# Optimization experiments

Measured on AMD Instinct MI355X. Metric: run time of the kernel, lower is better.

The kernel has to match this reference:

```python
import jax, jax.numpy as jnp
import numpy as np

N = 2048      # number of nodes (batch_size in original code)
D = 128       # node feature dim (fea_shape)
R = 43        # number of relation types (rel_weight = Linear(43, 1))


def setup_inputs() -> dict:
    key = jax.random.key(0)
    ks = jax.random.split(key, 9)
    inputs   = jax.random.normal(ks[0], (N, D), dtype=jnp.float32)
    relation = jax.random.normal(ks[1], (N, N, R), dtype=jnp.float32)
    rel_mask = jax.random.normal(ks[2], (N, N), dtype=jnp.float32)
    s_rel  = 1.0 / np.sqrt(R)
    s_feat = 1.0 / np.sqrt(D)
    w_rel  = jax.random.uniform(ks[3], (R, 1), jnp.float32, -s_rel, s_rel)
    b_rel  = jax.random.uniform(ks[4], (1,),   jnp.float32, -s_rel, s_rel)
    w_head = jax.random.uniform(ks[5], (D, 1), jnp.float32, -s_feat, s_feat)
    b_head = jax.random.uniform(ks[6], (1,),   jnp.float32, -s_feat, s_feat)
    w_tail = jax.random.uniform(ks[7], (D, 1), jnp.float32, -s_feat, s_feat)
    b_tail = jax.random.uniform(ks[8], (1,),   jnp.float32, -s_feat, s_feat)
    return dict(inputs=inputs, relation=relation, rel_mask=rel_mask,
                w_rel=w_rel, b_rel=b_rel, w_head=w_head, b_head=b_head,
                w_tail=w_tail, b_tail=b_tail)


def reference(inputs, relation, rel_mask, w_rel, b_rel, w_head, b_head, w_tail, b_tail):
    # rel_weight = Linear(43,1)(relation)[:, :, -1]  -> [N, N]
    rel_w = jnp.einsum('ijr,r->ij', relation, w_rel[:, 0]) + b_rel[0]
    # head @ ones^T + ones @ tail^T  == broadcast outer-sum  -> [N, N]
    head = inputs @ w_head + b_head          # [N, 1]
    tail = inputs @ w_tail + b_tail          # [N, 1]
    weight = head + tail.T + rel_w           # [N, N]
    # masked softmax over dim=0 (rows), then weighted aggregation
    weight_masked = jax.nn.softmax(rel_mask + weight, axis=0)
    return weight_masked @ inputs            # [N, D]
```

## Files before the change

kernel.cpp:

```cpp
#include <hip/hip_runtime.h>
#include <math.h>

#define N 2048
#define D 128
#define R 43
#define SPLIT 8
#define CHUNKS 32

typedef const __attribute__((address_space(1))) void* as1_cptr;
typedef __attribute__((address_space(3))) void* as3_ptr;

__global__ __launch_bounds__(256) void k_headtail(
    const float* __restrict__ inputs,
    const float* __restrict__ w_head, const float* __restrict__ b_head,
    const float* __restrict__ w_tail, const float* __restrict__ b_tail,
    float* __restrict__ head, float* __restrict__ tail)
{
    const int t = threadIdx.x;
    const int row = blockIdx.x * 64 + (t >> 2);
    const int q = t & 3;
    const float4* rp = (const float4*)(inputs + (size_t)row * D + q * 32);
    const float4* wh = (const float4*)(w_head + q * 32);
    const float4* wt = (const float4*)(w_tail + q * 32);
    float h = 0.f, tl = 0.f;
    #pragma unroll
    for (int k = 0; k < 8; ++k) {
        float4 v = rp[k];
        float4 a = wh[k];
        float4 b = wt[k];
        h  += v.x * a.x + v.y * a.y + v.z * a.z + v.w * a.w;
        tl += v.x * b.x + v.y * b.y + v.z * b.z + v.w * b.w;
    }
    h  += __shfl_xor(h, 1);  h  += __shfl_xor(h, 2);
    tl += __shfl_xor(tl, 1); tl += __shfl_xor(tl, 2);
    if (q == 0) {
        head[row] = h  + b_head[0];
        tail[row] = tl + b_tail[0];
    }
}

__global__ __launch_bounds__(256) void k_scores(
    const float* __restrict__ rel, const float* __restrict__ rel_mask,
    const float* __restrict__ w_rel, const float* __restrict__ b_rel,
    const float* __restrict__ head, const float* __restrict__ tail,
    float* __restrict__ s)
{
    __shared__ float lds[2 * 256 * R];
    const int t    = threadIdx.x;
    const int lane = t & 63;
    const int wave = t >> 6;
    const int k0 = wave * 11;
    const int k1 = (wave == 3) ? 43 : (k0 + 11);

    float w[R];
    #pragma unroll
    for (int r = 0; r < R; ++r) w[r] = w_rel[r];
    const float brel = b_rel[0];

    char* lbase = (char*)lds;
    const int c0 = blockIdx.x * 64;

    {
        const char* src = (const char*)rel + (size_t)c0 * 44032;
        for (int k = k0; k < k1; ++k)
            __builtin_amdgcn_global_load_lds(
                (as1_cptr)(src + k * 1024 + lane * 16),
                (as3_ptr)(lbase + k * 1024), 16, 0, 0);
    }

    int cur = 0;
    for (int tt = 0; tt < 64; ++tt) {
        __syncthreads();

        if (tt < 63) {
            const char* src = (const char*)rel + (size_t)(c0 + tt + 1) * 44032;
            char* dst = lbase + (cur ^ 1) * 44032;
            for (int k = k0; k < k1; ++k)
                __builtin_amdgcn_global_load_lds(
                    (as1_cptr)(src + k * 1024 + lane * 16),
                    (as3_ptr)(dst + k * 1024), 16, 0, 0);
        }

        const size_t p = (size_t)(c0 + tt) * 256 + t;
        const int i = (int)(p >> 11);
        const int j = (int)(p & (N - 1));
        const float hd = head[i];
        const float tl = tail[j];
        const float mk = rel_mask[p];

        const float* b = lds + cur * (256 * R) + t * R;
        float a0 = 0.f, a1 = 0.f, a2 = 0.f, a3 = 0.f;
        #pragma unroll
        for (int r = 0; r < 40; r += 4) {
            a0 += b[r]     * w[r];
            a1 += b[r + 1] * w[r + 1];
            a2 += b[r + 2] * w[r + 2];
            a3 += b[r + 3] * w[r + 3];
        }
        a0 += b[40] * w[40];
        a1 += b[41] * w[41];
        a2 += b[42] * w[42];

        s[p] = brel + ((a0 + a1) + (a2 + a3)) + hd + tl + mk;
        cur ^= 1;
    }
}

__global__ __launch_bounds__(256) void k_colstats_part(
    const float* __restrict__ s, float* __restrict__ mpart, float* __restrict__ lpart)
{
    const int j = (blockIdx.x & 7) * 256 + threadIdx.x;
    const int c = blockIdx.x >> 3;
    const int i0 = c * 64;
    float mx = -1e30f;
    for (int i = i0; i < i0 + 64; ++i)
        mx = fmaxf(mx, s[(size_t)i * N + j]);
    float sum = 0.f;
    for (int i = i0; i < i0 + 64; ++i)
        sum += __expf(s[(size_t)i * N + j] - mx);
    mpart[c * N + j] = mx;
    lpart[c * N + j] = sum;
}

__global__ __launch_bounds__(256) void k_colstats_comb(
    const float* __restrict__ mpart, const float* __restrict__ lpart,
    float* __restrict__ m, float* __restrict__ rl)
{
    const int j = blockIdx.x * 256 + threadIdx.x;
    float mx = -1e30f;
    #pragma unroll 8
    for (int c = 0; c < CHUNKS; ++c)
        mx = fmaxf(mx, mpart[c * N + j]);
    float sum = 0.f;
    #pragma unroll 8
    for (int c = 0; c < CHUNKS; ++c)
        sum += lpart[c * N + j] * __expf(mpart[c * N + j] - mx);
    m[j]  = mx;
    rl[j] = 1.0f / sum;
}

__global__ __launch_bounds__(256) void k_agg(
    const float* __restrict__ s, const float* __restrict__ inputs,
    const float* __restrict__ m, const float* __restrict__ rl,
    float* __restrict__ part)
{
    __shared__ float bt[64 * D];
    __shared__ float at[64 * 65];
    const int t  = threadIdx.x;
    const int i0 = (blockIdx.x & 31) * 64;
    const int sp = blockIdx.x >> 5;
    const int tr = t >> 4;
    const int tc = t & 15;
    float acc[4][8];
    #pragma unroll
    for (int a = 0; a < 4; ++a)
        #pragma unroll
        for (int b = 0; b < 8; ++b) acc[a][b] = 0.f;

    for (int tt = 0; tt < 4; ++tt) {
        const int j0 = sp * 256 + tt * 64;
        #pragma unroll
        for (int k = 0; k < 8; ++k) {
            int idx4 = k * 256 + t;
            int jj = idx4 >> 5, d4 = idx4 & 31;
            float4 v = *(const float4*)&inputs[(size_t)(j0 + jj) * D + d4 * 4];
            float sc = rl[j0 + jj];
            v.x *= sc; v.y *= sc; v.z *= sc; v.w *= sc;
            *(float4*)&bt[idx4 * 4] = v;
        }
        #pragma unroll
        for (int k = 0; k < 16; ++k) {
            int idx = k * 256 + t;
            int r = idx >> 6, jj = idx & 63;
            float sv = s[(size_t)(i0 + r) * N + j0 + jj];
            at[r * 65 + jj] = __expf(sv - m[j0 + jj]);
        }
        __syncthreads();
        for (int jj = 0; jj < 64; ++jj) {
            float4 x = *(float4*)&bt[jj * D + tc * 8];
            float4 y = *(float4*)&bt[jj * D + tc * 8 + 4];
            #pragma unroll
            for (int rr = 0; rr < 4; ++rr) {
                float a = at[(tr * 4 + rr) * 65 + jj];
                acc[rr][0] += a * x.x; acc[rr][1] += a * x.y;
                acc[rr][2] += a * x.z; acc[rr][3] += a * x.w;
                acc[rr][4] += a * y.x; acc[rr][5] += a * y.y;
                acc[rr][6] += a * y.z; acc[rr][7] += a * y.w;
            }
        }
        __syncthreads();
    }
    #pragma unroll
    for (int rr = 0; rr < 4; ++rr) {
        size_t o = ((size_t)sp * N + i0 + tr * 4 + rr) * D + tc * 8;
        *(float4*)&part[o]     = make_float4(acc[rr][0], acc[rr][1], acc[rr][2], acc[rr][3]);
        *(float4*)&part[o + 4] = make_float4(acc[rr][4], acc[rr][5], acc[rr][6], acc[rr][7]);
    }
}

__global__ __launch_bounds__(256) void k_reduce(
    const float* __restrict__ part, float* __restrict__ out)
{
    int idx = blockIdx.x * 256 + threadIdx.x;
    float4 v = make_float4(0.f, 0.f, 0.f, 0.f);
    #pragma unroll
    for (int sp = 0; sp < SPLIT; ++sp) {
        float4 p = *(const float4*)&part[(size_t)sp * N * D + (size_t)idx * 4];
        v.x += p.x; v.y += p.y; v.z += p.z; v.w += p.w;
    }
    *(float4*)&out[(size_t)idx * 4] = v;
}

extern "C" void kernel_launch(void* const* d_in, const int* in_sizes, int n_in,
                              void* d_out, int out_size, void* d_ws, size_t ws_size,
                              hipStream_t stream) {
    const float* inputs   = (const float*)d_in[0];
    const float* relation = (const float*)d_in[1];
    const float* rel_mask = (const float*)d_in[2];
    const float* w_rel    = (const float*)d_in[3];
    const float* b_rel    = (const float*)d_in[4];
    const float* w_head   = (const float*)d_in[5];
    const float* b_head   = (const float*)d_in[6];
    const float* w_tail   = (const float*)d_in[7];
    const float* b_tail   = (const float*)d_in[8];
    float* out = (float*)d_out;

    float* ws    = (float*)d_ws;
    float* s     = ws;
    float* head  = ws + (size_t)N * N;
    float* tail  = head + N;
    float* m     = tail + N;
    float* rl    = m + N;
    float* part  = rl + N;
    float* mpart = part + (size_t)SPLIT * N * D;
    float* lpart = mpart + (size_t)CHUNKS * N;

    k_headtail<<<N / 64, 256, 0, stream>>>(inputs, w_head, b_head, w_tail, b_tail, head, tail);
    k_scores<<<256, 256, 0, stream>>>(relation, rel_mask, w_rel, b_rel, head, tail, s);
    k_colstats_part<<<8 * CHUNKS, 256, 0, stream>>>(s, mpart, lpart);
    k_colstats_comb<<<N / 256, 256, 0, stream>>>(mpart, lpart, m, rl);
    k_agg<<<32 * SPLIT, 256, 0, stream>>>(s, inputs, m, rl, part);
    k_reduce<<<(N * D / 4) / 256, 256, 0, stream>>>(part, out);
}
```

Baseline: 995.1 us.

## Replace persistent double-buffered score kernel with one-tile-per-block register staging

The relation-score kernel previously ran 256 persistent blocks, each looping over 64 tiles with double-buffered async global-to-LDS loads and a block barrier per tile. It now launches one block per 256 pairs (16384 blocks). Each wave loads its own 64-pair slice of relation into registers with coalesced float4 loads, writes it to a private LDS region, and computes the dot product with no block-wide synchronization. This removes the barrier and pipeline overhead and relies on many resident blocks to hide memory latency. In exchange it adds per-block launch cost and reloads w_rel for every block.

```diff
diff --git a/kernel.cpp b/kernel.cpp
--- a/kernel.cpp
+++ b/kernel.cpp
@@ -6,9 +6,6 @@
 #define R 43
 #define SPLIT 8
 #define CHUNKS 32
-
-typedef const __attribute__((address_space(1))) void* as1_cptr;
-typedef __attribute__((address_space(3))) void* as3_ptr;
 
 __global__ __launch_bounds__(256) void k_headtail(
     const float* __restrict__ inputs,
@@ -45,65 +42,56 @@
     const float* __restrict__ head, const float* __restrict__ tail,
     float* __restrict__ s)
 {
-    __shared__ float lds[2 * 256 * R];
+    __shared__ float lds[4 * 2752];
     const int t    = threadIdx.x;
     const int lane = t & 63;
     const int wave = t >> 6;
-    const int k0 = wave * 11;
-    const int k1 = (wave == 3) ? 43 : (k0 + 11);
 
     float w[R];
     #pragma unroll
     for (int r = 0; r < R; ++r) w[r] = w_rel[r];
     const float brel = b_rel[0];
 
-    char* lbase = (char*)lds;
-    const int c0 = blockIdx.x * 64;
-
-    {
-        const char* src = (const char*)rel + (size_t)c0 * 44032;
-        for (int k = k0; k < k1; ++k)
-            __builtin_amdgcn_global_load_lds(
-                (as1_cptr)(src + k * 1024 + lane * 16),
-                (as3_ptr)(lbase + k * 1024), 16, 0, 0);
-    }
-
-    int cur = 0;
-    for (int tt = 0; tt < 64; ++tt) {
-        __syncthreads();
-
-        if (tt < 63) {
-            const char* src = (const char*)rel + (size_t)(c0 + tt + 1) * 44032;
-            char* dst = lbase + (cur ^ 1) * 44032;
-            for (int k = k0; k < k1; ++k)
-                __builtin_amdgcn_global_load_lds(
-                    (as1_cptr)(src + k * 1024 + lane * 16),
-                    (as3_ptr)(dst + k * 1024), 16, 0, 0);
-        }
-
-        const size_t p = (size_t)(c0 + tt) * 256 + t;
-        const int i = (int)(p >> 11);
-        const int j = (int)(p & (N - 1));
-        const float hd = head[i];
-        const float tl = tail[j];
-        const float mk = rel_mask[p];
-
-        const float* b = lds + cur * (256 * R) + t * R;
-        float a0 = 0.f, a1 = 0.f, a2 = 0.f, a3 = 0.f;
-        #pragma unroll
-        for (int r = 0; r < 40; r += 4) {
-            a0 += b[r]     * w[r];
-            a1 += b[r + 1] * w[r + 1];
-            a2 += b[r + 2] * w[r + 2];
-            a3 += b[r + 3] * w[r + 3];
-        }
-        a0 += b[40] * w[40];
-        a1 += b[41] * w[41];
-        a2 += b[42] * w[42];
-
-        s[p] = brel + ((a0 + a1) + (a2 + a3)) + hd + tl + mk;
-        cur ^= 1;
-    }
+    const size_t pair0 = (size_t)blockIdx.x * 256 + wave * 64;
+    const char*  src   = (const char*)rel + pair0 * 172;
+    char*        sb    = (char*)(lds + wave * 2752);
+
+    float4 v[10];
+    float  x[3];
+    #pragma unroll
+    for (int k = 0; k < 10; ++k)
+        v[k] = *(const float4*)(src + k * 1024 + lane * 16);
+    #pragma unroll
+    for (int k = 0; k < 3; ++k)
+        x[k] = *(const float*)(src + 10240 + k * 256 + lane * 4);
+    #pragma unroll
+    for (int k = 0; k < 10; ++k)
+        *(float4*)(sb + k * 1024 + lane * 16) = v[k];
+    #pragma unroll
+    for (int k = 0; k < 3; ++k)
+        *(float*)(sb + 10240 + k * 256 + lane * 4) = x[k];
+
+    const size_t p = pair0 + lane;
+    const int i = (int)(p >> 11);
+    const int j = (int)(p & (N - 1));
+    const float hd = head[i];
+    const float tl = tail[j];
+    const float mk = rel_mask[p];
+
+    const float* b = (const float*)sb + lane * 43;
+    float a0 = 0.f, a1 = 0.f, a2 = 0.f, a3 = 0.f;
+    #pragma unroll
+    for (int r = 0; r < 40; r += 4) {
+        a0 += b[r]     * w[r];
+        a1 += b[r + 1] * w[r + 1];
+        a2 += b[r + 2] * w[r + 2];
+        a3 += b[r + 3] * w[r + 3];
+    }
+    a0 += b[40] * w[40];
+    a1 += b[41] * w[41];
+    a2 += b[42] * w[42];
+
+    s[p] = brel + ((a0 + a1) + (a2 + a3)) + hd + tl + mk;
 }
 
 __global__ __launch_bounds__(256) void k_colstats_part(
@@ -236,7 +224,7 @@
     float* lpart = mpart + (size_t)CHUNKS * N;
 
     k_headtail<<<N / 64, 256, 0, stream>>>(inputs, w_head, b_head, w_tail, b_tail, head, tail);
-    k_scores<<<256, 256, 0, stream>>>(relation, rel_mask, w_rel, b_rel, head, tail, s);
+    k_scores<<<(N * N) / 256, 256, 0, stream>>>(relation, rel_mask, w_rel, b_rel, head, tail, s);
     k_colstats_part<<<8 * CHUNKS, 256, 0, stream>>>(s, mpart, lpart);
     k_colstats_comb<<<N / 256, 256, 0, stream>>>(mpart, lpart, m, rl);
     k_agg<<<32 * SPLIT, 256, 0, stream>>>(s, inputs, m, rl, part);
```

Result: no change. 976.6 us (-1.9%).
